# Performance work log

Measured on AMD Instinct MI355X. Metric: run time of the kernel, lower is better.

The kernel has to match this reference:

```python
import jax, jax.numpy as jnp
import numpy as np

B, T, D, E, K = 4, 2048, 1024, 8, 2

def setup_inputs() -> dict:
    key = jax.random.key(0)
    ks = jax.random.split(key, 4)
    scale = 1.0 / np.sqrt(D)
    return {
        "input_feat": jax.random.normal(ks[0], (B, T, D), dtype=jnp.float32),
        "delta": jax.random.normal(ks[1], (B, T, D), dtype=jnp.float32),
        "gate_W": jax.random.normal(ks[2], (E, D), dtype=jnp.float32) * scale,
        "gate_b": jnp.zeros((E,), dtype=jnp.float32),
        "expert_W": jax.random.normal(ks[3], (E, D, D), dtype=jnp.float32) * scale,
        "expert_b": jnp.zeros((E, D), dtype=jnp.float32),
    }

def reference(input_feat, delta, gate_W, gate_b, expert_W, expert_b):
    # Gating: logits [B,T,E], top-k over experts, softmax over the k logits
    gate_logits = jnp.einsum("btd,ed->bte", input_feat, gate_W) + gate_b
    topk_vals, topk_idx = jax.lax.top_k(gate_logits, K)          # [B,T,K]
    topk_weights = jax.nn.softmax(topk_vals, axis=-1)            # [B,T,K]

    # Dense per-expert linear on delta: [B,T,D,E] (torch Linear: x @ W.T + b)
    expert_outputs = jnp.einsum("btd,efd->btfe", delta, expert_W) + expert_b.T

    # Gather top-k expert outputs and weighted-combine
    idx = jnp.broadcast_to(topk_idx[:, :, None, :], (B, T, D, K))
    topk_outputs = jnp.take_along_axis(expert_outputs, idx, axis=-1)  # [B,T,D,K]
    weighted_output = jnp.sum(topk_outputs * topk_weights[:, :, None, :], axis=-1)
    return weighted_output
```

## Files before the change

kernel.cpp:

```cpp
#include <hip/hip_runtime.h>
#include <stdint.h>

#define NTOK 8192
#define D 1024
#define E 8
#define BM 128
#define BN 128
#define BK 64

typedef __attribute__((ext_vector_type(8))) short short8;
typedef __attribute__((ext_vector_type(4))) float f32x4;

__device__ __forceinline__ ushort f2bf(float f) {
  uint32_t x = __float_as_uint(f);
  x += 0x7FFFu + ((x >> 16) & 1u);
  return (ushort)(x >> 16);
}

#define NW4 2097152
#define ND4 2097152
#define NO4 2097152
#define CONV_BLOCKS ((NW4 + ND4 + NO4) / 256)
#define GATE_BLOCKS (NTOK / 4)

__global__ __launch_bounds__(256) void fused_pre_kernel(
    const float* __restrict__ expert_W, const float* __restrict__ delta,
    const float* __restrict__ x, const float* __restrict__ gW,
    const float* __restrict__ gb,
    ushort* __restrict__ Wb, ushort* __restrict__ Db,
    float* __restrict__ out, int* __restrict__ cnt,
    int* __restrict__ idx01, float2* __restrict__ w01) {
  int b = blockIdx.x;
  if (b < CONV_BLOCKS) {
    int i = b * 256 + threadIdx.x;
    if (i < E) cnt[i] = 0;
    if (i < NW4) {
      float4 v = ((const float4*)expert_W)[i];
      ushort4 u; u.x = f2bf(v.x); u.y = f2bf(v.y); u.z = f2bf(v.z); u.w = f2bf(v.w);
      ((ushort4*)Wb)[i] = u;
    } else if (i < NW4 + ND4) {
      int j = i - NW4;
      float4 v = ((const float4*)delta)[j];
      ushort4 u; u.x = f2bf(v.x); u.y = f2bf(v.y); u.z = f2bf(v.z); u.w = f2bf(v.w);
      ((ushort4*)Db)[j] = u;
    } else {
      ((float4*)out)[i - NW4 - ND4] = (float4){0.f, 0.f, 0.f, 0.f};
    }
    return;
  }
  int wave = threadIdx.x >> 6;
  int lane = threadIdx.x & 63;
  int t = (b - CONV_BLOCKS) * 4 + wave;

  const float4* xr = (const float4*)(x + (size_t)t * D) + lane * 4;
  float acc[E];
#pragma unroll
  for (int e = 0; e < E; ++e) acc[e] = 0.f;
#pragma unroll
  for (int q = 0; q < 4; ++q) {
    float4 xv = xr[q];
#pragma unroll
    for (int e = 0; e < E; ++e) {
      float4 wv = ((const float4*)(gW + e * D))[lane * 4 + q];
      acc[e] += xv.x * wv.x + xv.y * wv.y + xv.z * wv.z + xv.w * wv.w;
    }
  }
#pragma unroll
  for (int e = 0; e < E; ++e) {
    float v = acc[e];
#pragma unroll
    for (int off = 32; off > 0; off >>= 1) v += __shfl_xor(v, off, 64);
    acc[e] = v;
  }
  if (lane == 0) {
    float lg[E];
#pragma unroll
    for (int e = 0; e < E; ++e) lg[e] = acc[e] + gb[e];
    int i0 = 0; float v0 = lg[0];
#pragma unroll
    for (int e = 1; e < E; ++e) { if (lg[e] > v0) { v0 = lg[e]; i0 = e; } }
    int i1 = -1; float v1 = -1e30f;
#pragma unroll
    for (int e = 0; e < E; ++e) { if (e != i0 && lg[e] > v1) { v1 = lg[e]; i1 = e; } }
    float e1 = __expf(v1 - v0);
    float inv = 1.f / (1.f + e1);
    idx01[t] = i0 | (i1 << 16);
    w01[t] = make_float2(inv, e1 * inv);
  }
}

__global__ __launch_bounds__(256) void bin_kernel(
    const int* __restrict__ idx01, const float2* __restrict__ w01,
    int* __restrict__ cnt, int* __restrict__ list, float* __restrict__ wlist) {
  __shared__ int hist[E];
  __shared__ int base[E];
  int tid = threadIdx.x;
  int t = blockIdx.x * 256 + tid;
  if (tid < E) hist[tid] = 0;
  __syncthreads();

  int packed = idx01[t];
  float2 w = w01[t];
  int i0 = packed & 0xFFFF, i1 = packed >> 16;
  int r0 = atomicAdd(&hist[i0], 1);
  int r1 = atomicAdd(&hist[i1], 1);
  __syncthreads();
  if (tid < E) base[tid] = atomicAdd(&cnt[tid], hist[tid]);
  __syncthreads();

  int s0 = base[i0] + r0;
  list[i0 * NTOK + s0] = t; wlist[i0 * NTOK + s0] = w.x;
  int s1 = base[i1] + r1;
  list[i1 * NTOK + s1] = t; wlist[i1 * NTOK + s1] = w.y;
}

__global__ __launch_bounds__(256, 4) void moe_gemm_kernel(
    const ushort* __restrict__ Db, const ushort* __restrict__ Wb,
    const float* __restrict__ eb, const int* __restrict__ cnt,
    const int* __restrict__ list, const float* __restrict__ wlist,
    float* __restrict__ out) {
  int bx = blockIdx.x;
  int e = bx & 7;
  int nt = (bx >> 3) & 7;
  int mt = bx >> 6;
  int M = cnt[e];
  int m0 = mt * BM;
  if (m0 >= M) return;
  int n0 = nt * BN;

  __shared__ ushort As[BM * BK];
  __shared__ ushort Bs[BN * BK];

  int tid = threadIdx.x;
  int wave = tid >> 6;
  int lane = tid & 63;
  int wm = wave >> 1;
  int wn = wave & 1;
  const int c = lane & 15;
  const int q = lane >> 4;

  const int* listE = list + e * NTOK;

  int rloc = lane >> 3;
  int gglob = (lane & 7) ^ rloc;
  const ushort* aptr[4];
  ushort* alds[4];
#pragma unroll
  for (int p = 0; p < 4; ++p) {
    int r = m0 + wave * 32 + p * 8 + rloc;
    int tok = listE[r < M ? r : m0];
    aptr[p] = Db + (size_t)tok * D + gglob * 8;
    alds[p] = &As[(wave * 32 + p * 8) * BK];
  }
  const ushort* WbE = Wb + ((size_t)e << 20);
  const ushort* bptr[4];
  ushort* blds[4];
#pragma unroll
  for (int p = 0; p < 4; ++p) {
    int row = n0 + wave * 32 + p * 8 + rloc;
    bptr[p] = WbE + (size_t)row * D + gglob * 8;
    blds[p] = &Bs[(wave * 32 + p * 8) * BK];
  }

  f32x4 acc[4][4];
#pragma unroll
  for (int i = 0; i < 4; ++i)
#pragma unroll
    for (int j = 0; j < 4; ++j)
      acc[i][j] = (f32x4){0.f, 0.f, 0.f, 0.f};

  for (int k0 = 0; k0 < D; k0 += BK) {
#pragma unroll
    for (int p = 0; p < 4; ++p)
      __builtin_amdgcn_global_load_lds(
          (const __attribute__((address_space(1))) void*)(aptr[p] + k0),
          (__attribute__((address_space(3))) void*)alds[p], 16, 0, 0);
#pragma unroll
    for (int p = 0; p < 4; ++p)
      __builtin_amdgcn_global_load_lds(
          (const __attribute__((address_space(1))) void*)(bptr[p] + k0),
          (__attribute__((address_space(3))) void*)blds[p], 16, 0, 0);
    __syncthreads();

#pragma unroll
    for (int s = 0; s < 2; ++s) {
      int sw = (((s * 4 + q) ^ (c & 7)) * 8);
      short8 a[4], b[4];
#pragma unroll
      for (int i = 0; i < 4; ++i)
        a[i] = *(const short8*)&As[(wm * 64 + i * 16 + c) * BK + sw];
#pragma unroll
      for (int j = 0; j < 4; ++j)
        b[j] = *(const short8*)&Bs[(wn * 64 + j * 16 + c) * BK + sw];
#pragma unroll
      for (int i = 0; i < 4; ++i)
#pragma unroll
        for (int j = 0; j < 4; ++j)
          acc[i][j] = __builtin_amdgcn_mfma_f32_16x16x32_bf16(a[i], b[j], acc[i][j], 0, 0, 0);
    }
    __syncthreads();
  }

  float bias[4];
#pragma unroll
  for (int j = 0; j < 4; ++j)
    bias[j] = eb[e * D + n0 + wn * 64 + j * 16 + c];
  const float* wlE = wlist + e * NTOK;
#pragma unroll
  for (int i = 0; i < 4; ++i) {
#pragma unroll
    for (int r = 0; r < 4; ++r) {
      int m = m0 + wm * 64 + i * 16 + q * 4 + r;
      if (m < M) {
        int tok = listE[m];
        float w = wlE[m];
        float* orow = out + (size_t)tok * D + n0 + wn * 64 + c;
#pragma unroll
        for (int j = 0; j < 4; ++j)
          atomicAdd(&orow[j * 16], (acc[i][j][r] + bias[j]) * w);
      }
    }
  }
}

extern "C" void kernel_launch(void* const* d_in, const int* in_sizes, int n_in,
                              void* d_out, int out_size, void* d_ws, size_t ws_size,
                              hipStream_t stream) {
  const float* input_feat = (const float*)d_in[0];
  const float* delta      = (const float*)d_in[1];
  const float* gate_W     = (const float*)d_in[2];
  const float* gate_b     = (const float*)d_in[3];
  const float* expert_W   = (const float*)d_in[4];
  const float* expert_b   = (const float*)d_in[5];
  float* out = (float*)d_out;

  char* ws = (char*)d_ws;
  ushort* Wb    = (ushort*)ws;
  ushort* Db    = (ushort*)(ws + 16777216);
  char*   meta  = ws + 2 * 16777216;
  int*    cnt   = (int*)meta;
  int*    list  = (int*)(meta + 256);
  float*  wlist = (float*)(meta + 256 + NTOK * E * 4);
  int*    idx01 = (int*)(meta + 256 + 2 * NTOK * E * 4);
  float2* w01   = (float2*)(meta + 256 + 2 * NTOK * E * 4 + NTOK * 4);

  fused_pre_kernel<<<CONV_BLOCKS + GATE_BLOCKS, 256, 0, stream>>>(
      expert_W, delta, input_feat, gate_W, gate_b, Wb, Db, out, cnt, idx01, w01);
  bin_kernel<<<NTOK / 256, 256, 0, stream>>>(idx01, w01, cnt, list, wlist);
  moe_gemm_kernel<<<(NTOK / BM) * 64, 256, 0, stream>>>(
      Db, Wb, expert_b, cnt, list, wlist, out);
}
```

Measured before the change: 266.5 us.

## Load MFMA operands directly from global memory with register double-buffering instead of LDS

The GEMM no longer stages A and B tiles through shared memory with global_load_lds and barriers. Each lane loads its own 16-byte operand fragments straight from global memory into registers, prefetching the next 32-wide K slice while the current one feeds the MFMAs. This removes the LDS traffic and the __syncthreads calls, but the waves in a block now fetch overlapping data separately, relying on L1/L2 to absorb it. The per-lane 16-byte reads are strided by row, which makes them poorly coalesced. The occupancy hint in launch_bounds is also dropped.

```diff
diff --git a/kernel.cpp b/kernel.cpp
--- a/kernel.cpp
+++ b/kernel.cpp
@@ -6,7 +6,6 @@
 #define E 8
 #define BM 128
 #define BN 128
-#define BK 64
 
 typedef __attribute__((ext_vector_type(8))) short short8;
 typedef __attribute__((ext_vector_type(4))) float f32x4;
@@ -114,7 +113,7 @@
   list[i1 * NTOK + s1] = t; wlist[i1 * NTOK + s1] = w.y;
 }
 
-__global__ __launch_bounds__(256, 4) void moe_gemm_kernel(
+__global__ __launch_bounds__(256) void moe_gemm_kernel(
     const ushort* __restrict__ Db, const ushort* __restrict__ Wb,
     const float* __restrict__ eb, const int* __restrict__ cnt,
     const int* __restrict__ list, const float* __restrict__ wlist,
@@ -128,9 +127,6 @@
   if (m0 >= M) return;
   int n0 = nt * BN;
 
-  __shared__ ushort As[BM * BK];
-  __shared__ ushort Bs[BN * BK];
-
   int tid = threadIdx.x;
   int wave = tid >> 6;
   int lane = tid & 63;
@@ -141,26 +137,18 @@
 
   const int* listE = list + e * NTOK;
 
-  int rloc = lane >> 3;
-  int gglob = (lane & 7) ^ rloc;
   const ushort* aptr[4];
-  ushort* alds[4];
-#pragma unroll
-  for (int p = 0; p < 4; ++p) {
-    int r = m0 + wave * 32 + p * 8 + rloc;
-    int tok = listE[r < M ? r : m0];
-    aptr[p] = Db + (size_t)tok * D + gglob * 8;
-    alds[p] = &As[(wave * 32 + p * 8) * BK];
+#pragma unroll
+  for (int i = 0; i < 4; ++i) {
+    int m = m0 + wm * 64 + i * 16 + c;
+    int tok = listE[m < M ? m : m0];
+    aptr[i] = Db + (size_t)tok * D + q * 8;
   }
   const ushort* WbE = Wb + ((size_t)e << 20);
   const ushort* bptr[4];
-  ushort* blds[4];
-#pragma unroll
-  for (int p = 0; p < 4; ++p) {
-    int row = n0 + wave * 32 + p * 8 + rloc;
-    bptr[p] = WbE + (size_t)row * D + gglob * 8;
-    blds[p] = &Bs[(wave * 32 + p * 8) * BK];
-  }
+#pragma unroll
+  for (int j = 0; j < 4; ++j)
+    bptr[j] = WbE + (size_t)(n0 + wn * 64 + j * 16 + c) * D + q * 8;
 
   f32x4 acc[4][4];
 #pragma unroll
@@ -169,36 +157,25 @@
     for (int j = 0; j < 4; ++j)
       acc[i][j] = (f32x4){0.f, 0.f, 0.f, 0.f};
 
-  for (int k0 = 0; k0 < D; k0 += BK) {
-#pragma unroll
-    for (int p = 0; p < 4; ++p)
-      __builtin_amdgcn_global_load_lds(
-          (const __attribute__((address_space(1))) void*)(aptr[p] + k0),
-          (__attribute__((address_space(3))) void*)alds[p], 16, 0, 0);
-#pragma unroll
-    for (int p = 0; p < 4; ++p)
-      __builtin_amdgcn_global_load_lds(
-          (const __attribute__((address_space(1))) void*)(bptr[p] + k0),
-          (__attribute__((address_space(3))) void*)blds[p], 16, 0, 0);
-    __syncthreads();
-
-#pragma unroll
-    for (int s = 0; s < 2; ++s) {
-      int sw = (((s * 4 + q) ^ (c & 7)) * 8);
-      short8 a[4], b[4];
-#pragma unroll
-      for (int i = 0; i < 4; ++i)
-        a[i] = *(const short8*)&As[(wm * 64 + i * 16 + c) * BK + sw];
+  short8 a[2][4], b[2][4];
+#pragma unroll
+  for (int i = 0; i < 4; ++i) a[0][i] = *(const short8*)(aptr[i]);
+#pragma unroll
+  for (int j = 0; j < 4; ++j) b[0][j] = *(const short8*)(bptr[j]);
+
+  for (int k0 = 0; k0 < D; k0 += 32) {
+    int cur = (k0 >> 5) & 1, nxt = cur ^ 1;
+    if (k0 + 32 < D) {
+#pragma unroll
+      for (int i = 0; i < 4; ++i) a[nxt][i] = *(const short8*)(aptr[i] + k0 + 32);
+#pragma unroll
+      for (int j = 0; j < 4; ++j) b[nxt][j] = *(const short8*)(bptr[j] + k0 + 32);
+    }
+#pragma unroll
+    for (int i = 0; i < 4; ++i)
 #pragma unroll
       for (int j = 0; j < 4; ++j)
-        b[j] = *(const short8*)&Bs[(wn * 64 + j * 16 + c) * BK + sw];
-#pragma unroll
-      for (int i = 0; i < 4; ++i)
-#pragma unroll
-        for (int j = 0; j < 4; ++j)
-          acc[i][j] = __builtin_amdgcn_mfma_f32_16x16x32_bf16(a[i], b[j], acc[i][j], 0, 0, 0);
-    }
-    __syncthreads();
+        acc[i][j] = __builtin_amdgcn_mfma_f32_16x16x32_bf16(a[cur][i], b[cur][j], acc[i][j], 0, 0, 0);
   }
 
   float bias[4];
```

After: 345.2 us. 29.5% more time.
